# Performance work log

Measured on AMD Instinct MI355X. Metric: run time of the kernel, lower is better.

Reference implementation:

```python
import jax, jax.numpy as jnp
import numpy as np

N = 50000      # nodes
E = 800000     # edges
EL = 100000    # label edges to score
F_IN = 128
H = 4          # heads
C = 64         # hidden per head
D = H * C      # 256, node width after each conv
NEG_SLOPE = 0.2


def setup_inputs():
    key = jax.random.key(0)
    ks = jax.random.split(key, 16)
    s = 0.05
    inp = {
        "x": jax.random.normal(ks[0], (N, F_IN), jnp.float32),
        "edge_index": jax.random.randint(ks[1], (2, E), 0, N, jnp.int64),
        "edge_label_index": jax.random.randint(ks[2], (2, EL), 0, N, jnp.int64),
        # GATConv layer 1: in 128 -> heads*hidden 256
        "W1": jax.random.normal(ks[3], (F_IN, D), jnp.float32) * s,
        "a_src1": jax.random.normal(ks[4], (H, C), jnp.float32) * s,
        "a_dst1": jax.random.normal(ks[5], (H, C), jnp.float32) * s,
        "b1": jnp.zeros((D,), jnp.float32),
        # GATConv layer 2: 256 -> 256
        "W2": jax.random.normal(ks[6], (D, D), jnp.float32) * s,
        "a_src2": jax.random.normal(ks[7], (H, C), jnp.float32) * s,
        "a_dst2": jax.random.normal(ks[8], (H, C), jnp.float32) * s,
        "b2": jnp.zeros((D,), jnp.float32),
        # scorer MLP: Linear(512->64), ReLU, Linear(64->1)
        "Ws1": jax.random.normal(ks[9], (2 * D, C), jnp.float32) * s,
        "bs1": jnp.zeros((C,), jnp.float32),
        "Ws2": jax.random.normal(ks[10], (C, 1), jnp.float32) * s,
        "bs2": jnp.zeros((1,), jnp.float32),
    }
    return inp


def gat_layer(x, W, a_src, a_dst, b, src, dst):
    # linear transform and split heads: [N, H, C]
    h = (x @ W).reshape(N, H, C)
    # per-node attention logits [N, H]
    al_src = jnp.einsum("nhc,hc->nh", h, a_src)
    al_dst = jnp.einsum("nhc,hc->nh", h, a_dst)
    # per-edge raw scores [Etot, H]
    e = jax.nn.leaky_relu(al_src[src] + al_dst[dst], NEG_SLOPE)
    # stable scatter-softmax over incoming edges of each dst node
    m = jax.ops.segment_max(e, dst, num_segments=N)  # finite: self-loops present
    p = jnp.exp(e - m[dst])
    denom = jax.ops.segment_sum(p, dst, num_segments=N)
    alpha = p / denom[dst]
    # weighted aggregation: [N, H, C] -> concat heads
    out = jax.ops.segment_sum(h[src] * alpha[..., None], dst, num_segments=N)
    return out.reshape(N, D) + b


def reference(x, edge_index, edge_label_index, W1, a_src1, a_dst1, b1,
              W2, a_src2, a_dst2, b2, Ws1, bs1, Ws2, bs2):
    # add self loops (PyG GATConv default)
    loop = jnp.arange(N, dtype=edge_index.dtype)
    src = jnp.concatenate([edge_index[0], loop])
    dst = jnp.concatenate([edge_index[1], loop])

    z = gat_layer(x, W1, a_src1, a_dst1, b1, src, dst)
    z = jax.nn.elu(z)  # dropout is identity in eval mode
    z = gat_layer(z, W2, a_src2, a_dst2, b2, src, dst)
    z = jax.nn.elu(z)

    # link scorer: gather endpoints, concat, 2-layer MLP
    hcat = jnp.concatenate([z[edge_label_index[0]], z[edge_label_index[1]]], axis=-1)
    hid = jax.nn.relu(hcat @ Ws1 + bs1)
    return (hid @ Ws2 + bs2).reshape(-1)
```

## Files before the change

### kernel.cpp

```cpp
#include <hip/hip_runtime.h>
#include <math.h>

#define F_IN 128
#define D 256
#define H 4
#define C 64
#define NEG_SLOPE 0.2f

typedef __attribute__((ext_vector_type(8))) unsigned short ushort8;
typedef __attribute__((ext_vector_type(8))) short short8;
typedef __attribute__((ext_vector_type(4))) float floatx4;

__device__ __forceinline__ float leaky(float x) {
  return (x >= 0.f) ? x : NEG_SLOPE * x;
}
__device__ __forceinline__ unsigned short f2bf(float f) {
  unsigned u = __float_as_uint(f);
  return (unsigned short)((u + 0x7fffu + ((u >> 16) & 1u)) >> 16);
}
__device__ __forceinline__ float bf2f(unsigned short s) {
  return __uint_as_float((unsigned)s << 16);
}
__device__ __forceinline__ float waveReduceSum(float v) {
#pragma unroll
  for (int off = 32; off > 0; off >>= 1) v += __shfl_xor(v, off, 64);
  return v;
}

template <bool BF16OUT>
__global__ __launch_bounds__(256) void gemm_mfma(
    const unsigned short* __restrict__ A, const unsigned short* __restrict__ Bt,
    void* __restrict__ Cout, int M, int K, int Ncol) {
  __shared__ unsigned short Alds[128][40];
  __shared__ unsigned short Blds[128][40];

  const int t = threadIdx.x;
  const int w = t >> 6;
  const int l = t & 63;
  const int bm = blockIdx.x * 128;
  const int bn = blockIdx.y * 128;

  const int m16 = l & 15;
  const int q = l >> 4;

  const int sr = t >> 1;
  const int sc = (t & 1) * 2;
  int agr = bm + sr; if (agr >= M) agr = M - 1;
  const int bgr = bn + sr;

  floatx4 acc[8][2] = {};

  for (int k0 = 0; k0 < K; k0 += 32) {
    const ushort8 a0 = *(const ushort8*)&A[(size_t)agr * K + k0 + sc * 8];
    const ushort8 a1 = *(const ushort8*)&A[(size_t)agr * K + k0 + (sc + 1) * 8];
    const ushort8 b0 = *(const ushort8*)&Bt[(size_t)bgr * K + k0 + sc * 8];
    const ushort8 b1 = *(const ushort8*)&Bt[(size_t)bgr * K + k0 + (sc + 1) * 8];
    *(ushort8*)&Alds[sr][sc * 8] = a0;
    *(ushort8*)&Alds[sr][(sc + 1) * 8] = a1;
    *(ushort8*)&Blds[sr][sc * 8] = b0;
    *(ushort8*)&Blds[sr][(sc + 1) * 8] = b1;
    __syncthreads();

    short8 bf[2];
#pragma unroll
    for (int nt = 0; nt < 2; ++nt)
      bf[nt] = *(const short8*)&Blds[w * 32 + nt * 16 + m16][q * 8];
#pragma unroll
    for (int mt = 0; mt < 8; ++mt) {
      const short8 af = *(const short8*)&Alds[mt * 16 + m16][q * 8];
      acc[mt][0] = __builtin_amdgcn_mfma_f32_16x16x32_bf16(af, bf[0], acc[mt][0], 0, 0, 0);
      acc[mt][1] = __builtin_amdgcn_mfma_f32_16x16x32_bf16(af, bf[1], acc[mt][1], 0, 0, 0);
    }
    __syncthreads();
  }

#pragma unroll
  for (int mt = 0; mt < 8; ++mt)
#pragma unroll
    for (int nt = 0; nt < 2; ++nt) {
      const int col = bn + w * 32 + nt * 16 + m16;
#pragma unroll
      for (int i = 0; i < 4; ++i) {
        const int row = bm + mt * 16 + q * 4 + i;
        if (row < M) {
          if (BF16OUT)
            ((unsigned short*)Cout)[(size_t)row * Ncol + col] = f2bf(acc[mt][nt][i]);
          else
            ((float*)Cout)[(size_t)row * Ncol + col] = acc[mt][nt][i];
        }
      }
    }
}

__global__ void cast_bf16(const float* __restrict__ src, unsigned short* __restrict__ dst,
                          int n) {
  const int i = blockIdx.x * 256 + threadIdx.x;
  if (i < n) dst[i] = f2bf(src[i]);
}

__global__ void prep_weights(const float* __restrict__ W1, const float* __restrict__ W2,
                             const float* __restrict__ Ws1,
                             unsigned short* __restrict__ W1t,
                             unsigned short* __restrict__ W2t,
                             unsigned short* __restrict__ BcT) {
  const int i = blockIdx.x * 256 + threadIdx.x;
  if (i < 256 * 128) {
    const int n = i >> 7, k = i & 127;
    W1t[i] = f2bf(W1[(size_t)k * 256 + n]);
  }
  if (i < 256 * 256) {
    const int n = i >> 8, k = i & 255;
    W2t[i] = f2bf(W2[(size_t)k * 256 + n]);
  }
  if (i < 128 * 256) {
    const int n = i >> 8, k = i & 255;
    const float v = (n < 64) ? Ws1[(size_t)k * 64 + n]
                             : Ws1[(size_t)(k + 256) * 64 + (n - 64)];
    BcT[i] = f2bf(v);
  }
}

__global__ __launch_bounds__(256) void logits_kernel(
    const unsigned short* __restrict__ hb, const float* __restrict__ a_src,
    const float* __restrict__ a_dst, float* __restrict__ al_src,
    float* __restrict__ al_dst, int N) {
  const int wave = threadIdx.x >> 6;
  const int lane = threadIdx.x & 63;
  const int half = lane >> 5;
  const int l32 = lane & 31;
  const int n = blockIdx.x * 8 + wave * 2 + half;
  if (n >= N) return;
  const int c8 = l32 * 8;
  const ushort8 hv = *(const ushort8*)&hb[(size_t)n * D + c8];
  float as[8], ad[8];
  *(float4*)&as[0] = *(const float4*)&a_src[c8];
  *(float4*)&as[4] = *(const float4*)&a_src[c8 + 4];
  *(float4*)&ad[0] = *(const float4*)&a_dst[c8];
  *(float4*)&ad[4] = *(const float4*)&a_dst[c8 + 4];
  float ps = 0.f, pd = 0.f;
#pragma unroll
  for (int i = 0; i < 8; ++i) {
    const float hf = bf2f(hv[i]);
    ps += hf * as[i];
    pd += hf * ad[i];
  }
  ps += __shfl_xor(ps, 1, 64); pd += __shfl_xor(pd, 1, 64);
  ps += __shfl_xor(ps, 2, 64); pd += __shfl_xor(pd, 2, 64);
  ps += __shfl_xor(ps, 4, 64); pd += __shfl_xor(pd, 4, 64);
  if ((l32 & 7) == 0) {
    const int h = l32 >> 3;
    al_src[n * H + h] = ps;
    al_dst[n * H + h] = pd;
  }
}

__global__ void hist_kernel(const int* __restrict__ ei, int E, int N,
                            int* __restrict__ count) {
  const int e = blockIdx.x * blockDim.x + threadIdx.x;
  if (e >= E + N) return;
  const int d = (e < E) ? ei[E + e] : (e - E);
  atomicAdd(&count[d], 1);
}

__global__ __launch_bounds__(256) void scan_block(const int* __restrict__ in,
                                                  int* __restrict__ out,
                                                  int* __restrict__ blockSums, int n) {
  const int i = blockIdx.x * 256 + threadIdx.x;
  const int lane = threadIdx.x & 63;
  const int wid = threadIdx.x >> 6;
  const int val = (i < n) ? in[i] : 0;
  int incl = val;
#pragma unroll
  for (int off = 1; off < 64; off <<= 1) {
    int m = __shfl_up(incl, off, 64);
    if (lane >= off) incl += m;
  }
  __shared__ int wsum[4], woff[5];
  if (lane == 63) wsum[wid] = incl;
  __syncthreads();
  if (threadIdx.x == 0) {
    int s = 0;
    for (int w = 0; w < 4; ++w) { woff[w] = s; s += wsum[w]; }
    woff[4] = s;
  }
  __syncthreads();
  if (i < n) out[i] = incl - val + woff[wid];
  if (threadIdx.x == 0 && blockSums) blockSums[blockIdx.x] = woff[4];
}

__global__ void scan_add(int* __restrict__ data, const int* __restrict__ blockOff, int n) {
  const int i = blockIdx.x * 256 + threadIdx.x;
  if (i < n) data[i] += blockOff[blockIdx.x];
}

__global__ void scatter_kernel(const int* __restrict__ ei, int E, int N,
                               const int* __restrict__ rowptr,
                               int* __restrict__ fill, int* __restrict__ esrc) {
  const int e = blockIdx.x * blockDim.x + threadIdx.x;
  if (e >= E + N) return;
  int s, d;
  if (e < E) { s = ei[e]; d = ei[E + e]; } else { s = d = e - E; }
  const int pos = rowptr[d] + atomicAdd(&fill[d], 1);
  esrc[pos] = s;
}

__global__ void eal_prepass(const int* __restrict__ esrc, int Etot,
                            const float* __restrict__ al_src, float* __restrict__ eal) {
  const int i = blockIdx.x * 256 + threadIdx.x;
  if (i >= Etot) return;
  const float4 a = *(const float4*)&al_src[esrc[i] * 4];
  eal[i] = a.x;
  eal[Etot + i] = a.y;
  eal[2 * Etot + i] = a.z;
  eal[3 * Etot + i] = a.w;
}

__global__ __launch_bounds__(256) void agg_wave_kernel(
    const int* __restrict__ rowptr, const int* __restrict__ count,
    const int* __restrict__ esrc, int Etot, const float* __restrict__ eal,
    const float* __restrict__ al_dst, const unsigned short* __restrict__ hb,
    const float* __restrict__ bias, unsigned short* __restrict__ out, int N) {
  const int wave = threadIdx.x >> 6;
  const int d = blockIdx.x * 4 + wave;
  if (d >= N) return;
  const int lane = threadIdx.x & 63;
  const int base = rowptr[d];
  const int cnt = count[d];
  const float4 ald4 = *(const float4*)&al_dst[d * 4];

  const int hl = lane >> 4;
  const float aldA = ((const float*)&ald4)[hl];
  const float* __restrict__ ealA = eal + (size_t)hl * Etot + base;
  float sm = 0.f;
  for (int i = (lane & 15); i < cnt; i += 16) sm += __expf(leaky(ealA[i] + aldA));
  sm += __shfl_xor(sm, 1, 64);
  sm += __shfl_xor(sm, 2, 64);
  sm += __shfl_xor(sm, 4, 64);
  sm += __shfl_xor(sm, 8, 64);
  const float inv = 1.f / sm;

  const int half = lane >> 5;
  const int l32 = lane & 31;
  const int c8 = l32 * 8;
  const int ch = l32 >> 3;
  const float invB = __shfl(inv, ch * 16, 64);
  const float aldB = ((const float*)&ald4)[ch];
  const float* __restrict__ ealB = eal + (size_t)ch * Etot + base;
  const int* __restrict__ es = esrc + base;

  float acc[8] = {};
  for (int j = half; j < cnt; j += 2) {
    const int s = es[j];
    const float a = __expf(leaky(ealB[j] + aldB)) * invB;
    const ushort8 hv = *(const ushort8*)&hb[(size_t)s * D + c8];
#pragma unroll
    for (int i = 0; i < 8; ++i) acc[i] += bf2f(hv[i]) * a;
  }
#pragma unroll
  for (int i = 0; i < 8; ++i) acc[i] += __shfl_xor(acc[i], 32, 64);
  if (half == 0) {
    ushort8 o;
#pragma unroll
    for (int i = 0; i < 8; ++i) {
      const float v = acc[i] + bias[c8 + i];
      o[i] = f2bf((v > 0.f) ? v : expm1f(v));
    }
    *(ushort8*)&out[(size_t)d * D + c8] = o;
  }
}

__global__ __launch_bounds__(256) void score_kernel(
    const int* __restrict__ eli, int EL, const float* __restrict__ PQ,
    const float* __restrict__ bs1, const float* __restrict__ Ws2,
    const float* __restrict__ bs2, float* __restrict__ out) {
  const int e = blockIdx.x * 4 + (threadIdx.x >> 6);
  if (e >= EL) return;
  const int lane = threadIdx.x & 63;
  const int a = eli[e];
  const int b = eli[EL + e];
  float p = PQ[(size_t)a * 128 + lane] + PQ[(size_t)b * 128 + 64 + lane] + bs1[lane];
  p = (p > 0.f) ? p : 0.f;
  const float sum = waveReduceSum(p * Ws2[lane]);
  if (lane == 0) out[e] = sum + bs2[0];
}

extern "C" void kernel_launch(void* const* d_in, const int* in_sizes, int n_in,
                              void* d_out, int out_size, void* d_ws, size_t ws_size,
                              hipStream_t stream) {
  const float* x   = (const float*)d_in[0];
  const int*   ei  = (const int*)d_in[1];
  const int*   eli = (const int*)d_in[2];
  const float* W1  = (const float*)d_in[3];
  const float* as1 = (const float*)d_in[4];
  const float* ad1 = (const float*)d_in[5];
  const float* b1  = (const float*)d_in[6];
  const float* W2  = (const float*)d_in[7];
  const float* as2 = (const float*)d_in[8];
  const float* ad2 = (const float*)d_in[9];
  const float* b2  = (const float*)d_in[10];
  const float* Ws1 = (const float*)d_in[11];
  const float* bs1 = (const float*)d_in[12];
  const float* Ws2 = (const float*)d_in[13];
  const float* bs2 = (const float*)d_in[14];

  const int N = in_sizes[0] / F_IN;
  const int E = in_sizes[1] / 2;
  const int EL = in_sizes[2] / 2;
  const int Etot = E + N;

  unsigned short* hb = (unsigned short*)d_ws;
  unsigned short* zb = hb + (size_t)N * D;
  unsigned short* xb = zb + (size_t)N * D;
  unsigned short* W1t = xb + (size_t)N * F_IN;
  unsigned short* W2t = W1t + 256 * 128;
  unsigned short* BcT = W2t + 256 * 256;
  float* PQ     = (float*)(BcT + 128 * 256);
  float* al_src = PQ + (size_t)N * 128;
  float* al_dst = al_src + (size_t)N * H;
  float* eal    = al_dst + (size_t)N * H;
  int* count  = (int*)(eal + (size_t)4 * Etot);
  int* rowptr = count + N;
  int* fill   = rowptr + N;
  int* blockSums = fill + N;
  int* blockOff  = blockSums + 256;
  int* esrc   = blockOff + 256;

  const int edgeBlocks = (Etot + 255) / 256;
  const int nb = (N + 255) / 256;
  const dim3 gridLayer((N + 127) / 128, D / 128);
  const dim3 gridScore((N + 127) / 128, 1);

  hipMemsetAsync(count, 0, (size_t)N * sizeof(int), stream);
  hipMemsetAsync(fill, 0, (size_t)N * sizeof(int), stream);
  hist_kernel<<<edgeBlocks, 256, 0, stream>>>(ei, E, N, count);
  scan_block<<<nb, 256, 0, stream>>>(count, rowptr, blockSums, N);
  scan_block<<<1, 256, 0, stream>>>(blockSums, blockOff, nullptr, nb);
  scan_add<<<nb, 256, 0, stream>>>(rowptr, blockOff, N);
  scatter_kernel<<<edgeBlocks, 256, 0, stream>>>(ei, E, N, rowptr, fill, esrc);
  cast_bf16<<<(N * F_IN + 255) / 256, 256, 0, stream>>>(x, xb, N * F_IN);
  prep_weights<<<256, 256, 0, stream>>>(W1, W2, Ws1, W1t, W2t, BcT);

  gemm_mfma<true><<<gridLayer, 256, 0, stream>>>(xb, W1t, hb, N, F_IN, D);
  logits_kernel<<<(N + 7) / 8, 256, 0, stream>>>(hb, as1, ad1, al_src, al_dst, N);
  eal_prepass<<<edgeBlocks, 256, 0, stream>>>(esrc, Etot, al_src, eal);
  agg_wave_kernel<<<(N + 3) / 4, 256, 0, stream>>>(rowptr, count, esrc, Etot, eal,
                                                   al_dst, hb, b1, zb, N);

  gemm_mfma<true><<<gridLayer, 256, 0, stream>>>(zb, W2t, hb, N, D, D);
  logits_kernel<<<(N + 7) / 8, 256, 0, stream>>>(hb, as2, ad2, al_src, al_dst, N);
  eal_prepass<<<edgeBlocks, 256, 0, stream>>>(esrc, Etot, al_src, eal);
  agg_wave_kernel<<<(N + 3) / 4, 256, 0, stream>>>(rowptr, count, esrc, Etot, eal,
                                                   al_dst, hb, b2, zb, N);

  gemm_mfma<false><<<gridScore, 256, 0, stream>>>(zb, BcT, PQ, N, D, 128);
  score_kernel<<<(EL + 3) / 4, 256, 0, stream>>>(eli, EL, PQ, bs1, Ws2, bs2,
                                                 (float*)d_out);
}
```

Before: 505.0 us.

## Fuse bf16 cast into first GEMM and edge-logit gather into aggregation

The first GEMM now reads fp32 x directly and converts to bf16 while staging into LDS, which removes the separate cast kernel and its intermediate buffer. The eal_prepass kernel is also removed: the aggregation kernel gathers al_src per edge itself, computes all four heads' exp scores in one pass, and caches the first 64 edge weights per node in shared memory for reuse in the weighted sum. Nodes with more than 64 incoming edges recompute the gather and exp for the remaining edges. This trades extra random gathers for fewer kernel launches and less intermediate memory traffic.

After: 464.2 us. 1.09x faster.

```diff
diff --git a/kernel.cpp b/kernel.cpp
--- a/kernel.cpp
+++ b/kernel.cpp
@@ -27,9 +27,9 @@
   return v;
 }
 
-template <bool BF16OUT>
+template <bool AFP32, bool BF16OUT>
 __global__ __launch_bounds__(256) void gemm_mfma(
-    const unsigned short* __restrict__ A, const unsigned short* __restrict__ Bt,
+    const void* __restrict__ Ain, const unsigned short* __restrict__ Bt,
     void* __restrict__ Cout, int M, int K, int Ncol) {
   __shared__ unsigned short Alds[128][40];
   __shared__ unsigned short Blds[128][40];
@@ -51,14 +51,31 @@
   floatx4 acc[8][2] = {};
 
   for (int k0 = 0; k0 < K; k0 += 32) {
-    const ushort8 a0 = *(const ushort8*)&A[(size_t)agr * K + k0 + sc * 8];
-    const ushort8 a1 = *(const ushort8*)&A[(size_t)agr * K + k0 + (sc + 1) * 8];
-    const ushort8 b0 = *(const ushort8*)&Bt[(size_t)bgr * K + k0 + sc * 8];
-    const ushort8 b1 = *(const ushort8*)&Bt[(size_t)bgr * K + k0 + (sc + 1) * 8];
-    *(ushort8*)&Alds[sr][sc * 8] = a0;
-    *(ushort8*)&Alds[sr][(sc + 1) * 8] = a1;
-    *(ushort8*)&Blds[sr][sc * 8] = b0;
-    *(ushort8*)&Blds[sr][(sc + 1) * 8] = b1;
+    if (AFP32) {
+      const float* Af = (const float*)Ain;
+      float av[16];
+      *(float4*)&av[0]  = *(const float4*)&Af[(size_t)agr * K + k0 + sc * 8];
+      *(float4*)&av[4]  = *(const float4*)&Af[(size_t)agr * K + k0 + sc * 8 + 4];
+      *(float4*)&av[8]  = *(const float4*)&Af[(size_t)agr * K + k0 + (sc + 1) * 8];
+      *(float4*)&av[12] = *(const float4*)&Af[(size_t)agr * K + k0 + (sc + 1) * 8 + 4];
+      ushort8 a0, a1;
+#pragma unroll
+      for (int i = 0; i < 8; ++i) { a0[i] = f2bf(av[i]); a1[i] = f2bf(av[8 + i]); }
+      *(ushort8*)&Alds[sr][sc * 8] = a0;
+      *(ushort8*)&Alds[sr][(sc + 1) * 8] = a1;
+    } else {
+      const unsigned short* Ab = (const unsigned short*)Ain;
+      const ushort8 a0 = *(const ushort8*)&Ab[(size_t)agr * K + k0 + sc * 8];
+      const ushort8 a1 = *(const ushort8*)&Ab[(size_t)agr * K + k0 + (sc + 1) * 8];
+      *(ushort8*)&Alds[sr][sc * 8] = a0;
+      *(ushort8*)&Alds[sr][(sc + 1) * 8] = a1;
+    }
+    {
+      const ushort8 b0 = *(const ushort8*)&Bt[(size_t)bgr * K + k0 + sc * 8];
+      const ushort8 b1 = *(const ushort8*)&Bt[(size_t)bgr * K + k0 + (sc + 1) * 8];
+      *(ushort8*)&Blds[sr][sc * 8] = b0;
+      *(ushort8*)&Blds[sr][(sc + 1) * 8] = b1;
+    }
     __syncthreads();
 
     short8 bf[2];
@@ -90,12 +107,6 @@
         }
       }
     }
-}
-
-__global__ void cast_bf16(const float* __restrict__ src, unsigned short* __restrict__ dst,
-                          int n) {
-  const int i = blockIdx.x * 256 + threadIdx.x;
-  if (i < n) dst[i] = f2bf(src[i]);
 }
 
 __global__ void prep_weights(const float* __restrict__ W1, const float* __restrict__ W2,
@@ -204,20 +215,9 @@
   esrc[pos] = s;
 }
 
-__global__ void eal_prepass(const int* __restrict__ esrc, int Etot,
-                            const float* __restrict__ al_src, float* __restrict__ eal) {
-  const int i = blockIdx.x * 256 + threadIdx.x;
-  if (i >= Etot) return;
-  const float4 a = *(const float4*)&al_src[esrc[i] * 4];
-  eal[i] = a.x;
-  eal[Etot + i] = a.y;
-  eal[2 * Etot + i] = a.z;
-  eal[3 * Etot + i] = a.w;
-}
-
 __global__ __launch_bounds__(256) void agg_wave_kernel(
     const int* __restrict__ rowptr, const int* __restrict__ count,
-    const int* __restrict__ esrc, int Etot, const float* __restrict__ eal,
+    const int* __restrict__ esrc, const float* __restrict__ al_src,
     const float* __restrict__ al_dst, const unsigned short* __restrict__ hb,
     const float* __restrict__ bias, unsigned short* __restrict__ out, int N) {
   const int wave = threadIdx.x >> 6;
@@ -227,34 +227,55 @@
   const int base = rowptr[d];
   const int cnt = count[d];
   const float4 ald4 = *(const float4*)&al_dst[d * 4];
-
-  const int hl = lane >> 4;
-  const float aldA = ((const float*)&ald4)[hl];
-  const float* __restrict__ ealA = eal + (size_t)hl * Etot + base;
-  float sm = 0.f;
-  for (int i = (lane & 15); i < cnt; i += 16) sm += __expf(leaky(ealA[i] + aldA));
-  sm += __shfl_xor(sm, 1, 64);
-  sm += __shfl_xor(sm, 2, 64);
-  sm += __shfl_xor(sm, 4, 64);
-  sm += __shfl_xor(sm, 8, 64);
-  const float inv = 1.f / sm;
+  const int* __restrict__ es = esrc + base;
+
+  __shared__ float walpha[4][4][64];
+
+  float s0 = 0.f, s1 = 0.f, s2 = 0.f, s3 = 0.f;
+  for (int i = lane; i < cnt; i += 64) {
+    const float4 a = *(const float4*)&al_src[es[i] * 4];
+    const float e0 = __expf(leaky(a.x + ald4.x));
+    const float e1 = __expf(leaky(a.y + ald4.y));
+    const float e2 = __expf(leaky(a.z + ald4.z));
+    const float e3 = __expf(leaky(a.w + ald4.w));
+    s0 += e0; s1 += e1; s2 += e2; s3 += e3;
+    if (i < 64) {
+      walpha[wave][0][i] = e0;
+      walpha[wave][1][i] = e1;
+      walpha[wave][2][i] = e2;
+      walpha[wave][3][i] = e3;
+    }
+  }
+#pragma unroll
+  for (int off = 32; off > 0; off >>= 1) {
+    s0 += __shfl_xor(s0, off, 64);
+    s1 += __shfl_xor(s1, off, 64);
+    s2 += __shfl_xor(s2, off, 64);
+    s3 += __shfl_xor(s3, off, 64);
+  }
+  const float inv4[4] = {1.f / s0, 1.f / s1, 1.f / s2, 1.f / s3};
 
   const int half = lane >> 5;
   const int l32 = lane & 31;
   const int c8 = l32 * 8;
   const int ch = l32 >> 3;
-  const float invB = __shfl(inv, ch * 16, 64);
+  const float invB = inv4[ch];
   const float aldB = ((const float*)&ald4)[ch];
-  const float* __restrict__ ealB = eal + (size_t)ch * Etot + base;
-  const int* __restrict__ es = esrc + base;
 
   float acc[8] = {};
   for (int j = half; j < cnt; j += 2) {
     const int s = es[j];
-    const float a = __expf(leaky(ealB[j] + aldB)) * invB;
+    float wgt;
+    if (j < 64) {
+      wgt = walpha[wave][ch][j];
+    } else {
+      const float4 a = *(const float4*)&al_src[s * 4];
+      wgt = __expf(leaky(((const float*)&a)[ch] + aldB));
+    }
+    const float alpha = wgt * invB;
     const ushort8 hv = *(const ushort8*)&hb[(size_t)s * D + c8];
 #pragma unroll
-    for (int i = 0; i < 8; ++i) acc[i] += bf2f(hv[i]) * a;
+    for (int i = 0; i < 8; ++i) acc[i] += bf2f(hv[i]) * alpha;
   }
 #pragma unroll
   for (int i = 0; i < 8; ++i) acc[i] += __shfl_xor(acc[i], 32, 64);
@@ -310,15 +331,13 @@
 
   unsigned short* hb = (unsigned short*)d_ws;
   unsigned short* zb = hb + (size_t)N * D;
-  unsigned short* xb = zb + (size_t)N * D;
-  unsigned short* W1t = xb + (size_t)N * F_IN;
+  unsigned short* W1t = zb + (size_t)N * D;
   unsigned short* W2t = W1t + 256 * 128;
   unsigned short* BcT = W2t + 256 * 256;
   float* PQ     = (float*)(BcT + 128 * 256);
   float* al_src = PQ + (size_t)N * 128;
   float* al_dst = al_src + (size_t)N * H;
-  float* eal    = al_dst + (size_t)N * H;
-  int* count  = (int*)(eal + (size_t)4 * Etot);
+  int* count  = (int*)(al_dst + (size_t)N * H);
   int* rowptr = count + N;
   int* fill   = rowptr + N;
   int* blockSums = fill + N;
@@ -337,22 +356,19 @@
   scan_block<<<1, 256, 0, stream>>>(blockSums, blockOff, nullptr, nb);
   scan_add<<<nb, 256, 0, stream>>>(rowptr, blockOff, N);
   scatter_kernel<<<edgeBlocks, 256, 0, stream>>>(ei, E, N, rowptr, fill, esrc);
-  cast_bf16<<<(N * F_IN + 255) / 256, 256, 0, stream>>>(x, xb, N * F_IN);
   prep_weights<<<256, 256, 0, stream>>>(W1, W2, Ws1, W1t, W2t, BcT);
 
-  gemm_mfma<true><<<gridLayer, 256, 0, stream>>>(xb, W1t, hb, N, F_IN, D);
+  gemm_mfma<true, true><<<gridLayer, 256, 0, stream>>>(x, W1t, hb, N, F_IN, D);
   logits_kernel<<<(N + 7) / 8, 256, 0, stream>>>(hb, as1, ad1, al_src, al_dst, N);
-  eal_prepass<<<edgeBlocks, 256, 0, stream>>>(esrc, Etot, al_src, eal);
-  agg_wave_kernel<<<(N + 3) / 4, 256, 0, stream>>>(rowptr, count, esrc, Etot, eal,
+  agg_wave_kernel<<<(N + 3) / 4, 256, 0, stream>>>(rowptr, count, esrc, al_src,
                                                    al_dst, hb, b1, zb, N);
 
-  gemm_mfma<true><<<gridLayer, 256, 0, stream>>>(zb, W2t, hb, N, D, D);
+  gemm_mfma<false, true><<<gridLayer, 256, 0, stream>>>(zb, W2t, hb, N, D, D);
   logits_kernel<<<(N + 7) / 8, 256, 0, stream>>>(hb, as2, ad2, al_src, al_dst, N);
-  eal_prepass<<<edgeBlocks, 256, 0, stream>>>(esrc, Etot, al_src, eal);
-  agg_wave_kernel<<<(N + 3) / 4, 256, 0, stream>>>(rowptr, count, esrc, Etot, eal,
+  agg_wave_kernel<<<(N + 3) / 4, 256, 0, stream>>>(rowptr, count, esrc, al_src,
                                                    al_dst, hb, b2, zb, N);
 
-  gemm_mfma<false><<<gridScore, 256, 0, stream>>>(zb, BcT, PQ, N, D, 128);
+  gemm_mfma<false, false><<<gridScore, 256, 0, stream>>>(zb, BcT, PQ, N, D, 128);
   score_kernel<<<(EL + 3) / 4, 256, 0, stream>>>(eli, EL, PQ, bs1, Ws2, bs2,
                                                  (float*)d_out);
 }
```
